# Performance work log

Hardware: AMD Instinct MI355X
Metric: run time of the kernel (lower is better)

Reference implementation:

```python
import jax, jax.numpy as jnp
import numpy as np

B, T, DIN, DOUT, RANK = 4, 1, 4096, 11008, 512


def setup_inputs() -> dict:
    key = jax.random.key(0)
    ks = jax.random.split(key, 7)
    inp = jax.random.normal(ks[0], (B, T, DIN), jnp.float32)
    weight = jax.random.normal(ks[1], (DOUT, DIN), jnp.float32) * (1.0 / np.sqrt(DIN))
    bias = jax.random.normal(ks[2], (DOUT,), jnp.float32) * 0.02
    U = jax.random.normal(ks[3], (DOUT, RANK), jnp.float32) * (1.0 / np.sqrt(RANK))
    S = jax.random.uniform(ks[4], (RANK,), jnp.float32, 0.1, 1.0)
    V = jax.random.normal(ks[5], (DIN, RANK), jnp.float32) * (1.0 / np.sqrt(DIN))
    scale = jax.random.uniform(ks[6], (DIN,), jnp.float32, 0.5, 1.5)
    threshold = jnp.full((1,), 0.674, jnp.float32)
    return {"input": inp, "weight": weight, "bias": bias, "U": U, "S": S,
            "V": V, "scale": scale, "threshold": threshold}


def reference(input, weight, bias, U, S, V, scale, threshold):
    # r_sparse mode, decoding path (num_tokens == 1)
    th = threshold[0]
    # mask from scaled magnitudes; piecewise-constant w.r.t. inputs
    s_mask = jax.lax.stop_gradient(
        (jnp.abs(input * scale[None, None, :]) > th).astype(input.dtype))
    # sparse GEMM on masked input: [B,T,DIN] x [DOUT,DIN]^T + bias
    sparse_out = jnp.einsum('btd,od->bto', input * s_mask, weight) + bias
    # low-rank compensation on the complement: x @ (V diag(S)) @ U^T
    lr = jnp.einsum('btd,dr->btr', input * (1.0 - s_mask), V * S[None, :])
    lr = jnp.einsum('btr,or->bto', lr, U)
    return sparse_out + lr
```

## Files before the change

kernel.cpp:

```cpp
#include <hip/hip_runtime.h>
#include <cmath>

constexpr int DIN  = 4096;
constexpr int DOUT = 11008;
constexpr int RANK = 512;
constexpr int NB   = 4;

constexpr int NCHUNK = 256;
constexpr int DCH    = DIN / NCHUNK;
constexpr int SPLITK = 2;

__global__ __launch_bounds__(512)
void lr_partial_kernel(const float* __restrict__ x,
                       const float* __restrict__ scale,
                       const float* __restrict__ thp,
                       const float* __restrict__ V,
                       float* __restrict__ partial,
                       float* __restrict__ xs)
{
    __shared__ float xc[NB * DCH];
    const int chunk = blockIdx.x;
    const int t = threadIdx.x;
    const float th = thp[0];
    if (t < NB * DCH) {
        const int b = t / DCH, dd = t % DCH;
        const int d = chunk * DCH + dd;
        const float xv = x[b * DIN + d];
        const bool keep = fabsf(xv * scale[d]) > th;
        xc[t] = keep ? 0.f : xv;
        xs[b * DIN + d] = keep ? xv : 0.f;
    }
    __syncthreads();
    const int r = t;
    float a0 = 0.f, a1 = 0.f, a2 = 0.f, a3 = 0.f;
    #pragma unroll
    for (int dd = 0; dd < DCH; ++dd) {
        const float v = V[(size_t)(chunk * DCH + dd) * RANK + r];
        a0 = fmaf(xc[0 * DCH + dd], v, a0);
        a1 = fmaf(xc[1 * DCH + dd], v, a1);
        a2 = fmaf(xc[2 * DCH + dd], v, a2);
        a3 = fmaf(xc[3 * DCH + dd], v, a3);
    }
    float* p = partial + (size_t)chunk * (NB * RANK) + r;
    p[0 * RANK] = a0;
    p[1 * RANK] = a1;
    p[2 * RANK] = a2;
    p[3 * RANK] = a3;
}

__global__ __launch_bounds__(256)
void lr_reduce_kernel(const float* __restrict__ partial,
                      const float* __restrict__ S,
                      float* __restrict__ lr)
{
    const int t = blockIdx.x * 256 + threadIdx.x;
    const int idx = t >> 4;
    const int s = t & 15;
    float sum = 0.f;
    #pragma unroll
    for (int j = 0; j < 16; ++j)
        sum += partial[(size_t)(s * 16 + j) * (NB * RANK) + idx];
    #pragma unroll
    for (int m = 8; m >= 1; m >>= 1)
        sum += __shfl_xor(sum, m, 64);
    if (s == 0)
        lr[idx] = sum * S[idx & (RANK - 1)];
}

__global__ __launch_bounds__(256)
void rsparse_main_kernel(const float* __restrict__ xs,
                         const float* __restrict__ W,
                         const float* __restrict__ U,
                         const float* __restrict__ lr,
                         float* __restrict__ part)
{
    const int tid  = threadIdx.x;
    const int wave = tid >> 6, lane = tid & 63;
    const int pair = blockIdx.x * 2 + (wave >> 1);
    const int kh   = wave & 1;
    const int o0 = pair * 2, o1 = o0 + 1;
    const int kbase = kh * (DIN / SPLITK / 4);

    const float4* __restrict__ W0 = (const float4*)(W + (size_t)o0 * DIN);
    const float4* __restrict__ W1 = (const float4*)(W + (size_t)o1 * DIN);
    const float4* __restrict__ XS = (const float4*)xs;

    float acc0[NB] = {0.f, 0.f, 0.f, 0.f};
    float acc1[NB] = {0.f, 0.f, 0.f, 0.f};

    #pragma unroll 4
    for (int k = 0; k < 8; ++k) {
        const int c = kbase + (k << 6) + lane;
        const float4 w0 = W0[c];
        const float4 w1 = W1[c];
        #pragma unroll
        for (int b = 0; b < NB; ++b) {
            const float4 xv = XS[b * 1024 + c];
            acc0[b] = fmaf(w0.x, xv.x, acc0[b]);
            acc0[b] = fmaf(w0.y, xv.y, acc0[b]);
            acc0[b] = fmaf(w0.z, xv.z, acc0[b]);
            acc0[b] = fmaf(w0.w, xv.w, acc0[b]);
            acc1[b] = fmaf(w1.x, xv.x, acc1[b]);
            acc1[b] = fmaf(w1.y, xv.y, acc1[b]);
            acc1[b] = fmaf(w1.z, xv.z, acc1[b]);
            acc1[b] = fmaf(w1.w, xv.w, acc1[b]);
        }
    }

    if (kh == 0) {
        const float4* __restrict__ U0 = (const float4*)(U + (size_t)o0 * RANK);
        const float4* __restrict__ U1 = (const float4*)(U + (size_t)o1 * RANK);
        const float4* __restrict__ LR = (const float4*)lr;
        #pragma unroll
        for (int j = 0; j < 2; ++j) {
            const int c = (j << 6) + lane;
            const float4 u0 = U0[c];
            const float4 u1 = U1[c];
            #pragma unroll
            for (int b = 0; b < NB; ++b) {
                const float4 lv = LR[b * 128 + c];
                acc0[b] = fmaf(u0.x, lv.x, acc0[b]);
                acc0[b] = fmaf(u0.y, lv.y, acc0[b]);
                acc0[b] = fmaf(u0.z, lv.z, acc0[b]);
                acc0[b] = fmaf(u0.w, lv.w, acc0[b]);
                acc1[b] = fmaf(u1.x, lv.x, acc1[b]);
                acc1[b] = fmaf(u1.y, lv.y, acc1[b]);
                acc1[b] = fmaf(u1.z, lv.z, acc1[b]);
                acc1[b] = fmaf(u1.w, lv.w, acc1[b]);
            }
        }
    }

    #pragma unroll
    for (int b = 0; b < NB; ++b) {
        #pragma unroll
        for (int m = 32; m >= 1; m >>= 1) {
            acc0[b] += __shfl_xor(acc0[b], m, 64);
            acc1[b] += __shfl_xor(acc1[b], m, 64);
        }
    }

    if (lane == 0) {
        float* p = part + (size_t)kh * (NB * DOUT);
        #pragma unroll
        for (int b = 0; b < NB; ++b) {
            p[b * DOUT + o0] = acc0[b];
            p[b * DOUT + o1] = acc1[b];
        }
    }
}

__global__ __launch_bounds__(256)
void final_add_kernel(const float* __restrict__ part,
                      const float* __restrict__ bias,
                      float* __restrict__ out)
{
    const int i = blockIdx.x * 256 + threadIdx.x;
    const int o = i % DOUT;
    out[i] = part[i] + part[NB * DOUT + i] + bias[o];
}

extern "C" void kernel_launch(void* const* d_in, const int* in_sizes, int n_in,
                              void* d_out, int out_size, void* d_ws, size_t ws_size,
                              hipStream_t stream)
{
    const float* x     = (const float*)d_in[0];
    const float* W     = (const float*)d_in[1];
    const float* bias  = (const float*)d_in[2];
    const float* U     = (const float*)d_in[3];
    const float* S     = (const float*)d_in[4];
    const float* V     = (const float*)d_in[5];
    const float* scale = (const float*)d_in[6];
    const float* thp   = (const float*)d_in[7];
    float* out = (float*)d_out;

    float* partial = (float*)d_ws;
    float* lr      = partial + (size_t)NCHUNK * NB * RANK;
    float* xs      = lr + NB * RANK;
    float* part    = xs + NB * DIN;

    lr_partial_kernel<<<NCHUNK, 512, 0, stream>>>(x, scale, thp, V, partial, xs);
    lr_reduce_kernel<<<(NB * RANK * 16) / 256, 256, 0, stream>>>(partial, S, lr);
    rsparse_main_kernel<<<DOUT / 4, 256, 0, stream>>>(xs, W, U, lr, part);
    final_add_kernel<<<(NB * DOUT) / 256, 256, 0, stream>>>(part, bias, out);
}
```

Measured before the change: 52.72 us.

## Stage weight rows into LDS with async global_load_lds double buffering

```diff
diff --git a/kernel.cpp b/kernel.cpp
--- a/kernel.cpp
+++ b/kernel.cpp
@@ -8,7 +8,17 @@
 
 constexpr int NCHUNK = 256;
 constexpr int DCH    = DIN / NCHUNK;
+
 constexpr int SPLITK = 2;
+constexpr int ROWS   = 8;
+constexpr int CHUNK  = 256;
+constexpr int CH4    = CHUNK / 4;
+constexpr int NCH    = DIN / SPLITK / CHUNK;
+
+#define GLOAD_LDS16(gsrc, ldst)                                                   \
+    __builtin_amdgcn_global_load_lds(                                             \
+        (const __attribute__((address_space(1))) void*)(gsrc),                    \
+        (__attribute__((address_space(3))) void*)(ldst), 16, 0, 0)
 
 __global__ __launch_bounds__(512)
 void lr_partial_kernel(const float* __restrict__ x,
@@ -74,28 +84,42 @@
                          const float* __restrict__ lr,
                          float* __restrict__ part)
 {
+    __shared__ float sbuf[2 * ROWS * CHUNK];
     const int tid  = threadIdx.x;
     const int wave = tid >> 6, lane = tid & 63;
-    const int pair = blockIdx.x * 2 + (wave >> 1);
-    const int kh   = wave & 1;
-    const int o0 = pair * 2, o1 = o0 + 1;
-    const int kbase = kh * (DIN / SPLITK / 4);
-
-    const float4* __restrict__ W0 = (const float4*)(W + (size_t)o0 * DIN);
-    const float4* __restrict__ W1 = (const float4*)(W + (size_t)o1 * DIN);
+    const int kh   = blockIdx.y;
+    const int o0   = blockIdx.x * ROWS;
+    const int kofs = kh * (DIN / SPLITK);
+    const int r0   = wave * 2, r1 = r0 + 1;
+
     const float4* __restrict__ XS = (const float4*)xs;
+    const int xbase4 = kofs / 4;
+
+    auto STAGE = [&](int buf, int c) {
+        const float* s0 = W + (size_t)(o0 + r0) * DIN + kofs + c * CHUNK + lane * 4;
+        const float* s1 = W + (size_t)(o0 + r1) * DIN + kofs + c * CHUNK + lane * 4;
+        GLOAD_LDS16(s0, &sbuf[buf * (ROWS * CHUNK) + r0 * CHUNK]);
+        GLOAD_LDS16(s1, &sbuf[buf * (ROWS * CHUNK) + r1 * CHUNK]);
+    };
 
     float acc0[NB] = {0.f, 0.f, 0.f, 0.f};
     float acc1[NB] = {0.f, 0.f, 0.f, 0.f};
 
-    #pragma unroll 4
-    for (int k = 0; k < 8; ++k) {
-        const int c = kbase + (k << 6) + lane;
-        const float4 w0 = W0[c];
-        const float4 w1 = W1[c];
+    STAGE(0, 0);
+    __syncthreads();
+
+    int cur = 0;
+    for (int c = 0; c < NCH; ++c) {
+        if (c + 1 < NCH)
+            STAGE(cur ^ 1, c + 1);
+
+        const float4* wb = (const float4*)&sbuf[cur * (ROWS * CHUNK)];
+        const float4 w0 = wb[r0 * CH4 + lane];
+        const float4 w1 = wb[r1 * CH4 + lane];
+        const int x4 = xbase4 + c * CH4 + lane;
         #pragma unroll
         for (int b = 0; b < NB; ++b) {
-            const float4 xv = XS[b * 1024 + c];
+            const float4 xv = XS[b * 1024 + x4];
             acc0[b] = fmaf(w0.x, xv.x, acc0[b]);
             acc0[b] = fmaf(w0.y, xv.y, acc0[b]);
             acc0[b] = fmaf(w0.z, xv.z, acc0[b]);
@@ -105,11 +129,14 @@
             acc1[b] = fmaf(w1.z, xv.z, acc1[b]);
             acc1[b] = fmaf(w1.w, xv.w, acc1[b]);
         }
+
+        __syncthreads();
+        cur ^= 1;
     }
 
     if (kh == 0) {
-        const float4* __restrict__ U0 = (const float4*)(U + (size_t)o0 * RANK);
-        const float4* __restrict__ U1 = (const float4*)(U + (size_t)o1 * RANK);
+        const float4* __restrict__ U0 = (const float4*)(U + (size_t)(o0 + r0) * RANK);
+        const float4* __restrict__ U1 = (const float4*)(U + (size_t)(o0 + r1) * RANK);
         const float4* __restrict__ LR = (const float4*)lr;
         #pragma unroll
         for (int j = 0; j < 2; ++j) {
@@ -144,8 +171,8 @@
         float* p = part + (size_t)kh * (NB * DOUT);
         #pragma unroll
         for (int b = 0; b < NB; ++b) {
-            p[b * DOUT + o0] = acc0[b];
-            p[b * DOUT + o1] = acc1[b];
+            p[b * DOUT + o0 + r0] = acc0[b];
+            p[b * DOUT + o0 + r1] = acc1[b];
         }
     }
 }
@@ -155,9 +182,17 @@
                       const float* __restrict__ bias,
                       float* __restrict__ out)
 {
-    const int i = blockIdx.x * 256 + threadIdx.x;
-    const int o = i % DOUT;
-    out[i] = part[i] + part[NB * DOUT + i] + bias[o];
+    const int i4 = blockIdx.x * 256 + threadIdx.x;
+    const int o4 = i4 % (DOUT / 4);
+    const float4 p0 = ((const float4*)part)[i4];
+    const float4 p1 = ((const float4*)part)[NB * DOUT / 4 + i4];
+    const float4 bv = ((const float4*)bias)[o4];
+    float4 r;
+    r.x = p0.x + p1.x + bv.x;
+    r.y = p0.y + p1.y + bv.y;
+    r.z = p0.z + p1.z + bv.z;
+    r.w = p0.w + p1.w + bv.w;
+    ((float4*)out)[i4] = r;
 }
 
 extern "C" void kernel_launch(void* const* d_in, const int* in_sizes, int n_in,
@@ -181,6 +216,8 @@
 
     lr_partial_kernel<<<NCHUNK, 512, 0, stream>>>(x, scale, thp, V, partial, xs);
     lr_reduce_kernel<<<(NB * RANK * 16) / 256, 256, 0, stream>>>(partial, S, lr);
-    rsparse_main_kernel<<<DOUT / 4, 256, 0, stream>>>(xs, W, U, lr, part);
-    final_add_kernel<<<(NB * DOUT) / 256, 256, 0, stream>>>(part, bias, out);
-}
+
+    dim3 grid(DOUT / ROWS, SPLITK);
+    rsparse_main_kernel<<<grid, 256, 0, stream>>>(xs, W, U, lr, part);
+    final_add_kernel<<<(NB * DOUT / 4) / 256, 256, 0, stream>>>(part, bias, out);
+}
```

Result: faster. 47.92 us (-9.1%).
